# Optimization experiments

Hardware: AMD Instinct MI355X
Metric: run time of the kernel (lower is better)

## Reference

```python
import jax, jax.numpy as jnp
import numpy as np

# -------- static graph construction (Traffic4cast-style pixel grid) --------
H, W = 495, 436
N = H * W                    # 215820 nodes
D_NODE, D_EDGE, UNITS = 128, 32, 128
UQ = UNITS // 4              # per-quadrant width (combination='concat')
SCALE = 1.0 / 4.0            # 1/(max_neighbors+1)

def _first_occ_unique(v):
    """tf.unique semantics: unique values in first-occurrence order + idx map."""
    u, first, inv = np.unique(v, return_index=True, return_inverse=True)
    order = np.argsort(first)
    rank = np.empty(len(u), dtype=np.int64)
    rank[order] = np.arange(len(u))
    return u[order], rank[inv]

def _build_graph():
    r, c = np.meshgrid(np.arange(H), np.arange(W), indexing='ij')
    node_loc = np.stack([r.ravel(), c.ravel()], -1).astype(np.int64)
    def grid_edges(r0, r1, c0, c1, dr, dc):
        rr, cc = np.meshgrid(np.arange(r0, r1), np.arange(c0, c1), indexing='ij')
        src = (rr * W + cc).ravel()
        dst = ((rr + dr) * W + (cc + dc)).ravel()
        return np.stack([src, dst], -1).astype(np.int64)
    eis = [grid_edges(1, H, 0, W, -1, 0),   # north
           grid_edges(0, H, 0, W - 1, 0, 1),# east
           grid_edges(0, H - 1, 0, W, 1, 0),# south
           grid_edges(0, H, 1, W, 0, -1)]   # west
    return node_loc, eis

NODE_LOC, EIS = _build_graph()

# --- graph_pooling_2x2 bucketing (col_idx=0): pos_id = (r//2)*half_cols + c//2 ---
_half_cols = NODE_LOC[:, 0].max() + 1
_pos_id = (NODE_LOC // 2 * np.array([_half_cols, 1])).sum(-1)
_, NEW_NODE_IDS = _first_occ_unique(_pos_id)
N_POOLED = int(NEW_NODE_IDS.max()) + 1

# --- remove_duplicate_edges precompute per direction (static, int-only) ---
EDGE_SEG, K_UNIQ, KEEP_IDX, NEW_EIDX = [], [], [], []
for _ei in EIS:
    _pe = NEW_NODE_IDS[_ei]
    _lin = _pe[:, 0] * N + _pe[:, 1]
    _u, _seg = _first_occ_unique(_lin)
    _ne = np.stack([_u // N, _u % N], -1)
    _keep = np.where(_ne[:, 0] != _ne[:, 1])[0]
    EDGE_SEG.append(_seg)
    K_UNIQ.append(len(_u))
    KEEP_IDX.append(_keep)
    NEW_EIDX.append(_ne[_keep])


def setup_inputs() -> dict:
    key = jax.random.key(0)
    ks = jax.random.split(key, 9)
    inp = {
        'x': jax.random.normal(ks[0], (N, D_NODE), dtype=jnp.float32),
        'node_loc': jnp.asarray(NODE_LOC),
        'edge_index_n': jnp.asarray(EIS[0]),
        'edge_index_e': jnp.asarray(EIS[1]),
        'edge_index_s': jnp.asarray(EIS[2]),
        'edge_index_w': jnp.asarray(EIS[3]),
        'edges_n': jax.random.uniform(ks[1], (EIS[0].shape[0], D_EDGE), dtype=jnp.float32),
        'edges_e': jax.random.uniform(ks[2], (EIS[1].shape[0], D_EDGE), dtype=jnp.float32),
        'edges_s': jax.random.uniform(ks[3], (EIS[2].shape[0], D_EDGE), dtype=jnp.float32),
        'edges_w': jax.random.uniform(ks[4], (EIS[3].shape[0], D_EDGE), dtype=jnp.float32),
        'W_emb': jax.random.normal(ks[5], (4, D_NODE, UQ), dtype=jnp.float32) * 0.05,
        'W_edge': jax.random.normal(ks[6], (4, D_EDGE + 2 * UQ, UQ), dtype=jnp.float32) * 0.05,
        'W_node': jax.random.normal(ks[7], (D_NODE + UNITS, UNITS), dtype=jnp.float32) * 0.05,
    }
    return inp


def reference(x, node_loc, edge_index_n, edge_index_e, edge_index_s, edge_index_w,
              edges_n, edges_e, edges_s, edges_w, W_emb, W_edge, W_node):
    n = x.shape[0]
    eis = (edge_index_n, edge_index_e, edge_index_s, edge_index_w)
    efs = (edges_n, edges_e, edges_s, edges_w)
    aggs, quad_edges = [], []
    # GeoQuadrantGCN.call_concat (use_global=False, use_bias=False, relu)
    for q in range(4):
        ei = eis[q]
        xq = jax.nn.relu(x @ W_emb[q])                              # [N, UQ]
        edge_in = jnp.concatenate([efs[q], xq[ei[:, 0]], xq[ei[:, 1]]], axis=-1)
        edge = jax.nn.relu(edge_in @ W_edge[q])                     # [E, UQ]
        aggs.append(jax.ops.segment_sum(edge, ei[:, 1], num_segments=n) * SCALE)
        quad_edges.append(edge)
    x2 = jax.nn.relu(jnp.concatenate([x] + aggs, axis=-1) @ W_node) # [N, UNITS]
    # graph_pooling_2x2
    x_pooled = jax.ops.segment_max(x2, jnp.asarray(NEW_NODE_IDS), num_segments=N_POOLED)
    new_pos = jax.ops.segment_min(node_loc // 2, jnp.asarray(NEW_NODE_IDS), num_segments=N_POOLED)
    new_efeats = [
        jax.ops.segment_max(quad_edges[q], jnp.asarray(EDGE_SEG[q]), num_segments=K_UNIQ[q])[KEEP_IDX[q]]
        for q in range(4)
    ]
    new_eidx = [jnp.asarray(NEW_EIDX[q]) for q in range(4)]
    return (x_pooled, new_pos, *new_eidx, *new_efeats)
```

## Files before the change

kernel.cpp:

```cpp
#include <hip/hip_runtime.h>

#define NN 215820
#define NPOOL 54064
#define KN 53846
#define KE 53816

static constexpr size_t OFF_POS = (size_t)NPOOL * 128;
static constexpr size_t OFF_EIN = OFF_POS + (size_t)NPOOL * 2;
static constexpr size_t OFF_EIE = OFF_EIN + (size_t)KN * 2;
static constexpr size_t OFF_EIS = OFF_EIE + (size_t)KE * 2;
static constexpr size_t OFF_EIW = OFF_EIS + (size_t)KN * 2;
static constexpr size_t OFF_EFN = OFF_EIW + (size_t)KE * 2;
static constexpr size_t OFF_EFE = OFF_EFN + (size_t)KN * 32;
static constexpr size_t OFF_EFS = OFF_EFE + (size_t)KE * 32;
static constexpr size_t OFF_EFW = OFF_EFS + (size_t)KN * 32;

typedef __attribute__((ext_vector_type(8))) short  short8v;
typedef __attribute__((ext_vector_type(4))) float  floatx4;

__device__ __align__(16) unsigned short g_wn_h[128 * 256];
__device__ __align__(16) unsigned short g_wn_l[128 * 256];
__device__ __align__(16) unsigned short g_we_h[128 * 128];
__device__ __align__(16) unsigned short g_we_l[128 * 128];

__device__ __forceinline__ void bf16split(float x, unsigned short& h,
                                          unsigned short& l) {
  const unsigned int u = __float_as_uint(x);
  h = (unsigned short)(u >> 16);
  const float hf = __uint_as_float(u & 0xffff0000u);
  l = (unsigned short)(__float_as_uint(x - hf) >> 16);
}

__global__ __launch_bounds__(256, 4) void k_xq(const float* __restrict__ x,
                                               float* __restrict__ xq) {
  __shared__ __align__(16) short As_h[128 * 32], As_l[128 * 32];
  __shared__ __align__(16) short Bs_h[128 * 32], Bs_l[128 * 32];
  const int t  = threadIdx.x;
  const int n0 = blockIdx.x * 128;
  const int srow = t >> 1, q0 = t & 1;
  int sn = n0 + srow; if (sn >= NN) sn = NN - 1;
  const float* srcx = x + (size_t)sn * 128;
  const int w = t >> 6, lane = t & 63;
  const int lr = lane & 15, lg = lane >> 4;

  floatx4 acc[2][8];
#pragma unroll
  for (int mi = 0; mi < 2; ++mi)
#pragma unroll
    for (int ni = 0; ni < 8; ++ni) acc[mi][ni] = (floatx4){0.f, 0.f, 0.f, 0.f};

  for (int ks = 0; ks < 4; ++ks) {
    __syncthreads();
#pragma unroll
    for (int cc = 0; cc < 2; ++cc) {
      const int q = q0 + 2 * cc;
      const floatx4 v0 = *(const floatx4*)(srcx + ks * 32 + q * 8);
      const floatx4 v1 = *(const floatx4*)(srcx + ks * 32 + q * 8 + 4);
      short8v hv, lv;
#pragma unroll
      for (int j = 0; j < 4; ++j) {
        unsigned short h, l;
        bf16split(v0[j], h, l); hv[j] = (short)h; lv[j] = (short)l;
        bf16split(v1[j], h, l); hv[4 + j] = (short)h; lv[4 + j] = (short)l;
      }
      const int off = srow * 64 + ((q * 16) ^ ((srow & 3) << 4));
      *(short8v*)((char*)As_h + off) = hv;
      *(short8v*)((char*)As_l + off) = lv;
      const size_t wb = (size_t)srow * 128 + ks * 32 + q * 8;
      *(short8v*)((char*)Bs_h + off) = *(const short8v*)(g_we_h + wb);
      *(short8v*)((char*)Bs_l + off) = *(const short8v*)(g_we_l + wb);
    }
    __syncthreads();
    short8v ah[2], al[2];
#pragma unroll
    for (int mi = 0; mi < 2; ++mi) {
      const int row = (mi ? 64 : 0) + 16 * w + lr;
      const int off = row * 64 + ((lg * 16) ^ ((row & 3) << 4));
      ah[mi] = *(const short8v*)((const char*)As_h + off);
      al[mi] = *(const short8v*)((const char*)As_l + off);
    }
#pragma unroll
    for (int ni = 0; ni < 8; ++ni) {
      const int col = 16 * ni + lr;
      const int off = col * 64 + ((lg * 16) ^ ((col & 3) << 4));
      const short8v bh = *(const short8v*)((const char*)Bs_h + off);
      const short8v bl = *(const short8v*)((const char*)Bs_l + off);
#pragma unroll
      for (int mi = 0; mi < 2; ++mi) {
        acc[mi][ni] = __builtin_amdgcn_mfma_f32_16x16x32_bf16(ah[mi], bh, acc[mi][ni], 0, 0, 0);
        acc[mi][ni] = __builtin_amdgcn_mfma_f32_16x16x32_bf16(ah[mi], bl, acc[mi][ni], 0, 0, 0);
        acc[mi][ni] = __builtin_amdgcn_mfma_f32_16x16x32_bf16(al[mi], bh, acc[mi][ni], 0, 0, 0);
      }
    }
  }
#pragma unroll
  for (int ni = 0; ni < 8; ++ni) {
    const int col = 16 * ni + lr;
    const int qq = col >> 5, u = col & 31;
#pragma unroll
    for (int mi = 0; mi < 2; ++mi) {
      const int nb = n0 + (mi ? 64 : 0) + 16 * w + 4 * lg;
#pragma unroll
      for (int r = 0; r < 4; ++r) {
        const int n = nb + r;
        if (n < NN)
          xq[((size_t)qq * NN + n) * 32 + u] = fmaxf(acc[mi][ni][r], 0.f);
      }
    }
  }
}

__global__ __launch_bounds__(256, 4) void k_node(const float* __restrict__ x,
                                                 const float* __restrict__ agg,
                                                 float* __restrict__ out) {
  __shared__ short As_h[128 * 32], As_l[128 * 32];
  __shared__ short Bs_h[128 * 32], Bs_l[128 * 32];
  const int t   = threadIdx.x;
  const int pr  = blockIdx.y;
  const int pc0 = blockIdx.x * 32;

  const int srow = t >> 1, q0 = t & 1;
  int ra = (srow < 64) ? 2 * pr : 2 * pr + 1; if (ra > 494) ra = 494;
  int ca = 2 * pc0 + (srow & 63);          if (ca > 435) ca = 435;
  const size_t snode = (size_t)ra * 436 + ca;

  const int w = t >> 6, lane = t & 63;
  const int lr = lane & 15, lg = lane >> 4;

  floatx4 acc[2][8];
#pragma unroll
  for (int mi = 0; mi < 2; ++mi)
#pragma unroll
    for (int ni = 0; ni < 8; ++ni) acc[mi][ni] = (floatx4){0.f, 0.f, 0.f, 0.f};

  for (int ks = 0; ks < 8; ++ks) {
    __syncthreads();
    const float* src = (ks < 4) ? (x + snode * 128 + ks * 32)
                                : (agg + snode * 128 + (ks - 4) * 32);
#pragma unroll
    for (int cc = 0; cc < 2; ++cc) {
      const int q = q0 + 2 * cc;
      const floatx4 v0 = *(const floatx4*)(src + q * 8);
      const floatx4 v1 = *(const floatx4*)(src + q * 8 + 4);
      short8v hv, lv;
#pragma unroll
      for (int j = 0; j < 4; ++j) {
        unsigned short h, l;
        bf16split(v0[j], h, l); hv[j] = (short)h; lv[j] = (short)l;
        bf16split(v1[j], h, l); hv[4 + j] = (short)h; lv[4 + j] = (short)l;
      }
      const int off = srow * 64 + ((q * 16) ^ ((srow & 3) << 4));
      *(short8v*)((char*)As_h + off) = hv;
      *(short8v*)((char*)As_l + off) = lv;
      const size_t wb = (size_t)srow * 256 + ks * 32 + q * 8;
      *(short8v*)((char*)Bs_h + off) = *(const short8v*)(g_wn_h + wb);
      *(short8v*)((char*)Bs_l + off) = *(const short8v*)(g_wn_l + wb);
    }
    __syncthreads();
    short8v ah[2], al[2];
#pragma unroll
    for (int mi = 0; mi < 2; ++mi) {
      const int row = (mi ? 64 : 0) + 16 * w + lr;
      const int off = row * 64 + ((lg * 16) ^ ((row & 3) << 4));
      ah[mi] = *(const short8v*)((const char*)As_h + off);
      al[mi] = *(const short8v*)((const char*)As_l + off);
    }
#pragma unroll
    for (int ni = 0; ni < 8; ++ni) {
      const int col = 16 * ni + lr;
      const int off = col * 64 + ((lg * 16) ^ ((col & 3) << 4));
      const short8v bh = *(const short8v*)((const char*)Bs_h + off);
      const short8v bl = *(const short8v*)((const char*)Bs_l + off);
#pragma unroll
      for (int mi = 0; mi < 2; ++mi) {
        acc[mi][ni] = __builtin_amdgcn_mfma_f32_16x16x32_bf16(ah[mi], bh, acc[mi][ni], 0, 0, 0);
        acc[mi][ni] = __builtin_amdgcn_mfma_f32_16x16x32_bf16(ah[mi], bl, acc[mi][ni], 0, 0, 0);
        acc[mi][ni] = __builtin_amdgcn_mfma_f32_16x16x32_bf16(al[mi], bh, acc[mi][ni], 0, 0, 0);
      }
    }
  }
#pragma unroll
  for (int ni = 0; ni < 8; ++ni) {
#pragma unroll
    for (int k = 0; k < 2; ++k) {
      float v = fmaxf(fmaxf(acc[0][ni][2 * k], acc[0][ni][2 * k + 1]),
                      fmaxf(acc[1][ni][2 * k], acc[1][ni][2 * k + 1]));
      v = fmaxf(v, 0.f);
      const int pc = pc0 + 8 * w + 2 * lg + k;
      if (pc < 218) out[((size_t)pr * 218 + pc) * 128 + 16 * ni + lr] = v;
    }
  }
}

__global__ __launch_bounds__(256) void k_edge(
    const float* __restrict__ ef_n, const float* __restrict__ ef_e,
    const float* __restrict__ ef_s, const float* __restrict__ ef_w,
    const float* __restrict__ xq, const float* __restrict__ W_edge,
    float* __restrict__ agg, float* __restrict__ out) {
  const int q = blockIdx.y;
  const float* ef; float* efb; int P;
  if (q == 0)      { ef = ef_n; P = 107692; efb = out + OFF_EFN; }
  else if (q == 1) { ef = ef_e; P = 107880; efb = out + OFF_EFE; }
  else if (q == 2) { ef = ef_s; P = 107692; efb = out + OFF_EFS; }
  else             { ef = ef_w; P = 107880; efb = out + OFF_EFW; }
  const int j = threadIdx.x & 31, slot = threadIdx.x >> 5;
  const float* Wq = W_edge + q * 3072;
  float wcol[96];
#pragma unroll
  for (int k = 0; k < 96; ++k) wcol[k] = Wq[k * 32 + j];
  const float* xqq = xq + (size_t)q * NN * 32;
  __shared__ float ein[8][192];
  float* row = ein[slot];

  for (int p = blockIdx.x * 8 + slot; p < P; p += gridDim.x * 8) {
    int e1, src1, dst1, e2, src2, dst2, kidx; bool kept, has2;
    if (q == 0) {
      const int rp = p / 218, pc = p - rp * 218;
      const int r = rp + 1, c = 2 * pc;
      e1 = (r - 1) * 436 + c; e2 = e1 + 1;
      src1 = r * 436 + c; dst1 = src1 - 436;
      src2 = src1 + 1; dst2 = dst1 + 1; has2 = true;
      kept = (r & 1) == 0; kidx = ((r >> 1) - 1) * 218 + pc;
    } else if (q == 2) {
      const int r = p / 218, pc = p - r * 218;
      const int c = 2 * pc;
      e1 = r * 436 + c; e2 = e1 + 1;
      src1 = e1; dst1 = src1 + 436;
      src2 = src1 + 1; dst2 = dst1 + 1; has2 = true;
      kept = (r & 1) == 1; kidx = (r >> 1) * 218 + pc;
    } else if (q == 1) {
      const int pr = p / 435, c = p - pr * 435;
      e1 = 2 * pr * 435 + c; e2 = e1 + 435;
      src1 = 2 * pr * 436 + c; dst1 = src1 + 1;
      src2 = src1 + 436; dst2 = dst1 + 436;
      has2 = pr < 247;
      kept = (c & 1) == 1; kidx = pr * 217 + (c >> 1);
    } else {
      const int pr = p / 435, cm = p - pr * 435;
      const int c = cm + 1;
      e1 = 2 * pr * 435 + cm; e2 = e1 + 435;
      src1 = 2 * pr * 436 + c; dst1 = src1 - 1;
      src2 = src1 + 436; dst2 = dst1 + 436;
      has2 = pr < 247;
      kept = (c & 1) == 0; kidx = pr * 217 + (c >> 1) - 1;
    }
    const int e2c = has2 ? e2 : e1;
    const int s2c = has2 ? src2 : src1;
    const int d2c = has2 ? dst2 : dst1;
    row[j]       = ef[(size_t)e1 * 32 + j];
    row[32 + j]  = xqq[(size_t)src1 * 32 + j];
    row[64 + j]  = xqq[(size_t)dst1 * 32 + j];
    row[96 + j]  = ef[(size_t)e2c * 32 + j];
    row[128 + j] = xqq[(size_t)s2c * 32 + j];
    row[160 + j] = xqq[(size_t)d2c * 32 + j];
    float a1 = 0.f, a2 = 0.f;
#pragma unroll
    for (int kq = 0; kq < 24; ++kq) {
      const float4 b1 = *(const float4*)&row[4 * kq];
      const float4 b2 = *(const float4*)&row[96 + 4 * kq];
      a1 = fmaf(b1.x, wcol[4 * kq + 0], a1); a1 = fmaf(b1.y, wcol[4 * kq + 1], a1);
      a1 = fmaf(b1.z, wcol[4 * kq + 2], a1); a1 = fmaf(b1.w, wcol[4 * kq + 3], a1);
      a2 = fmaf(b2.x, wcol[4 * kq + 0], a2); a2 = fmaf(b2.y, wcol[4 * kq + 1], a2);
      a2 = fmaf(b2.z, wcol[4 * kq + 2], a2); a2 = fmaf(b2.w, wcol[4 * kq + 3], a2);
    }
    const float f1 = fmaxf(a1, 0.f), f2 = fmaxf(a2, 0.f);
    agg[(size_t)dst1 * 128 + q * 32 + j] = f1 * 0.25f;
    if (has2) agg[(size_t)dst2 * 128 + q * 32 + j] = f2 * 0.25f;
    if (kept) efb[(size_t)kidx * 32 + j] = has2 ? fmaxf(f1, f2) : f1;
  }
}

__global__ __launch_bounds__(256) void k_misc(float* __restrict__ out,
                                              float* __restrict__ agg,
                                              const float* __restrict__ W_node,
                                              const float* __restrict__ W_emb) {
  int u = blockIdx.x * 256 + threadIdx.x;
  if (u < 436 * 32) {
    agg[((size_t)494 * 436 + (u >> 5)) * 128 + (u & 31)] = 0.f; return;
  }
  u -= 436 * 32;
  if (u < 495 * 32) {
    agg[(size_t)(u >> 5) * 436 * 128 + 32 + (u & 31)] = 0.f; return;
  }
  u -= 495 * 32;
  if (u < 436 * 32) {
    agg[(size_t)(u >> 5) * 128 + 64 + (u & 31)] = 0.f; return;
  }
  u -= 436 * 32;
  if (u < 495 * 32) {
    agg[((size_t)(u >> 5) * 436 + 435) * 128 + 96 + (u & 31)] = 0.f; return;
  }
  u -= 495 * 32;
  if (u < NPOOL * 2) {
    const int p  = u >> 1;
    const int pr = p / 218, pc = p - pr * 218;
    out[OFF_POS + u] = (float)((u & 1) ? pc : pr); return;
  }
  u -= NPOOL * 2;
  if (u < KN * 2) {
    const int e  = u >> 1;
    const int kr = e / 218 + 1, pc = e - (kr - 1) * 218;
    const int s  = kr * 218 + pc;
    out[OFF_EIN + u] = (float)((u & 1) ? (s - 218) : s); return;
  }
  u -= KN * 2;
  if (u < KE * 2) {
    const int e  = u >> 1;
    const int pr = e / 217, jj = e - pr * 217;
    const int s  = pr * 218 + jj;
    out[OFF_EIE + u] = (float)((u & 1) ? (s + 1) : s); return;
  }
  u -= KE * 2;
  if (u < KN * 2) {
    const int e  = u >> 1;
    const int k  = e / 218, pc = e - k * 218;
    const int s  = k * 218 + pc;
    out[OFF_EIS + u] = (float)((u & 1) ? (s + 218) : s); return;
  }
  u -= KN * 2;
  if (u < KE * 2) {
    const int e  = u >> 1;
    const int pr = e / 217, jj = e - pr * 217;
    const int s  = pr * 218 + jj + 1;
    out[OFF_EIW + u] = (float)((u & 1) ? (s - 1) : s); return;
  }
  u -= KE * 2;
  if (u < 256 * 128) {
    const int k = u >> 7, c = u & 127;
    unsigned short h, l;
    bf16split(W_node[u], h, l);
    g_wn_h[(size_t)c * 256 + k] = h;
    g_wn_l[(size_t)c * 256 + k] = l;
    return;
  }
  u -= 256 * 128;
  if (u < 4 * 128 * 32) {
    const int q = u >> 12, k = (u >> 5) & 127, uu = u & 31;
    unsigned short h, l;
    bf16split(W_emb[u], h, l);
    g_we_h[(size_t)(q * 32 + uu) * 128 + k] = h;
    g_we_l[(size_t)(q * 32 + uu) * 128 + k] = l;
  }
}

extern "C" void kernel_launch(void* const* d_in, const int* in_sizes, int n_in,
                              void* d_out, int out_size, void* d_ws, size_t ws_size,
                              hipStream_t stream) {
  const float* x      = (const float*)d_in[0];
  const float* ef_n   = (const float*)d_in[6];
  const float* ef_e   = (const float*)d_in[7];
  const float* ef_s   = (const float*)d_in[8];
  const float* ef_w   = (const float*)d_in[9];
  const float* W_emb  = (const float*)d_in[10];
  const float* W_edge = (const float*)d_in[11];
  const float* W_node = (const float*)d_in[12];
  float* out = (float*)d_out;

  float* xq  = (float*)d_ws;
  float* agg = xq + (size_t)NN * 128;

  const int misc_total = (436 + 495 + 436 + 495) * 32 + NPOOL * 2 +
                         2 * (KN * 2 + KE * 2) + 256 * 128 + 4 * 128 * 32;
  k_misc<<<dim3((misc_total + 255) / 256), 256, 0, stream>>>(out, agg,
                                                             W_node, W_emb);
  k_xq  <<<dim3((NN + 127) / 128), 256, 0, stream>>>(x, xq);
  k_edge<<<dim3(512, 4), 256, 0, stream>>>(ef_n, ef_e, ef_s, ef_w,
                                           xq, W_edge, agg, out);
  k_node<<<dim3(7, 248), 256, 0, stream>>>(x, agg, out);
}
```

Measured before the change: 467.0 us.

## Rewrite edge MLP as split-bf16 MFMA GEMM over spatial tiles

Replaces the scalar per-edge FMA loop in the edge kernel with a tiled 128x32x96 GEMM on MFMA. It splits fp32 into high and low bf16 halves and issues three products to keep near-fp32 accuracy. The W_edge matrix is pre-split into bf16 halves in the misc kernel. Edges are now tiled by grid rows and columns so gathers are contiguous and the pooled max is done in registers. This targets the FP32 ALU cost and the shared-memory row staging, at the price of more blocks, conversion work and redundant overlapping tiles at row ends.

Measured after the change: 448.8 us. 3.9% less time.

```diff
diff --git a/kernel.cpp b/kernel.cpp
--- a/kernel.cpp
+++ b/kernel.cpp
@@ -22,6 +22,8 @@
 __device__ __align__(16) unsigned short g_wn_l[128 * 256];
 __device__ __align__(16) unsigned short g_we_h[128 * 128];
 __device__ __align__(16) unsigned short g_we_l[128 * 128];
+__device__ __align__(16) unsigned short g_wd_h[128 * 96];
+__device__ __align__(16) unsigned short g_wd_l[128 * 96];
 
 __device__ __forceinline__ void bf16split(float x, unsigned short& h,
                                           unsigned short& l) {
@@ -192,88 +194,178 @@
   }
 }
 
-__global__ __launch_bounds__(256) void k_edge(
+__global__ __launch_bounds__(256, 4) void k_edge(
     const float* __restrict__ ef_n, const float* __restrict__ ef_e,
     const float* __restrict__ ef_s, const float* __restrict__ ef_w,
-    const float* __restrict__ xq, const float* __restrict__ W_edge,
-    float* __restrict__ agg, float* __restrict__ out) {
-  const int q = blockIdx.y;
-  const float* ef; float* efb; int P;
-  if (q == 0)      { ef = ef_n; P = 107692; efb = out + OFF_EFN; }
-  else if (q == 1) { ef = ef_e; P = 107880; efb = out + OFF_EFE; }
-  else if (q == 2) { ef = ef_s; P = 107692; efb = out + OFF_EFS; }
-  else             { ef = ef_w; P = 107880; efb = out + OFF_EFW; }
-  const int j = threadIdx.x & 31, slot = threadIdx.x >> 5;
-  const float* Wq = W_edge + q * 3072;
-  float wcol[96];
-#pragma unroll
-  for (int k = 0; k < 96; ++k) wcol[k] = Wq[k * 32 + j];
+    const float* __restrict__ xq, float* __restrict__ agg,
+    float* __restrict__ out) {
+  __shared__ __align__(16) short As_h[128 * 32], As_l[128 * 32];
+  __shared__ __align__(16) short Bs_h[32 * 32],  Bs_l[32 * 32];
+  const int t = threadIdx.x;
+  int b = blockIdx.x;
+
+  int q, row = 0, pr = 0, c0;
+  const float* ef; float* efb;
+  if (b < 1976)        { q = 0; ef = ef_n; efb = out + OFF_EFN;
+                         row = b >> 2; c0 = (b & 3) * 128; if (c0 > 308) c0 = 308; }
+  else if (b < 3952)   { b -= 1976; q = 2; ef = ef_s; efb = out + OFF_EFS;
+                         row = b >> 2; c0 = (b & 3) * 128; if (c0 > 308) c0 = 308; }
+  else if (b < 5688)   { b -= 3952; q = 1; ef = ef_e; efb = out + OFF_EFE;
+                         pr = b / 7;  c0 = (b - pr * 7) * 64; if (c0 > 371) c0 = 371; }
+  else                 { b -= 5688; q = 3; ef = ef_w; efb = out + OFF_EFW;
+                         pr = b / 7;  c0 = (b - pr * 7) * 64; if (c0 > 371) c0 = 371; }
   const float* xqq = xq + (size_t)q * NN * 32;
-  __shared__ float ein[8][192];
-  float* row = ein[slot];
-
-  for (int p = blockIdx.x * 8 + slot; p < P; p += gridDim.x * 8) {
-    int e1, src1, dst1, e2, src2, dst2, kidx; bool kept, has2;
-    if (q == 0) {
-      const int rp = p / 218, pc = p - rp * 218;
-      const int r = rp + 1, c = 2 * pc;
-      e1 = (r - 1) * 436 + c; e2 = e1 + 1;
-      src1 = r * 436 + c; dst1 = src1 - 436;
-      src2 = src1 + 1; dst2 = dst1 + 1; has2 = true;
-      kept = (r & 1) == 0; kidx = ((r >> 1) - 1) * 218 + pc;
-    } else if (q == 2) {
-      const int r = p / 218, pc = p - r * 218;
-      const int c = 2 * pc;
-      e1 = r * 436 + c; e2 = e1 + 1;
-      src1 = e1; dst1 = src1 + 436;
-      src2 = src1 + 1; dst2 = dst1 + 1; has2 = true;
-      kept = (r & 1) == 1; kidx = (r >> 1) * 218 + pc;
-    } else if (q == 1) {
-      const int pr = p / 435, c = p - pr * 435;
-      e1 = 2 * pr * 435 + c; e2 = e1 + 435;
-      src1 = 2 * pr * 436 + c; dst1 = src1 + 1;
-      src2 = src1 + 436; dst2 = dst1 + 436;
-      has2 = pr < 247;
-      kept = (c & 1) == 1; kidx = pr * 217 + (c >> 1);
+
+  const int srow = t >> 1, q0 = t & 1;
+  const float *base0, *base1, *base2;
+  if (q == 0) {
+    const int e = row * 436 + c0 + srow;
+    base0 = ef  + (size_t)e * 32;
+    base1 = xqq + (size_t)(e + 436) * 32;
+    base2 = xqq + (size_t)e * 32;
+  } else if (q == 2) {
+    const int e = row * 436 + c0 + srow;
+    base0 = ef  + (size_t)e * 32;
+    base1 = xqq + (size_t)e * 32;
+    base2 = xqq + (size_t)(e + 436) * 32;
+  } else {
+    int r = 2 * pr + (srow >> 6); if (r > 494) r = 494;
+    const int cc = c0 + (srow & 63);
+    if (q == 1) {
+      base0 = ef  + ((size_t)r * 435 + cc) * 32;
+      base1 = xqq + ((size_t)r * 436 + cc) * 32;
+      base2 = base1 + 32;
     } else {
-      const int pr = p / 435, cm = p - pr * 435;
-      const int c = cm + 1;
-      e1 = 2 * pr * 435 + cm; e2 = e1 + 435;
-      src1 = 2 * pr * 436 + c; dst1 = src1 - 1;
-      src2 = src1 + 436; dst2 = dst1 + 436;
-      has2 = pr < 247;
-      kept = (c & 1) == 0; kidx = pr * 217 + (c >> 1) - 1;
-    }
-    const int e2c = has2 ? e2 : e1;
-    const int s2c = has2 ? src2 : src1;
-    const int d2c = has2 ? dst2 : dst1;
-    row[j]       = ef[(size_t)e1 * 32 + j];
-    row[32 + j]  = xqq[(size_t)src1 * 32 + j];
-    row[64 + j]  = xqq[(size_t)dst1 * 32 + j];
-    row[96 + j]  = ef[(size_t)e2c * 32 + j];
-    row[128 + j] = xqq[(size_t)s2c * 32 + j];
-    row[160 + j] = xqq[(size_t)d2c * 32 + j];
-    float a1 = 0.f, a2 = 0.f;
-#pragma unroll
-    for (int kq = 0; kq < 24; ++kq) {
-      const float4 b1 = *(const float4*)&row[4 * kq];
-      const float4 b2 = *(const float4*)&row[96 + 4 * kq];
-      a1 = fmaf(b1.x, wcol[4 * kq + 0], a1); a1 = fmaf(b1.y, wcol[4 * kq + 1], a1);
-      a1 = fmaf(b1.z, wcol[4 * kq + 2], a1); a1 = fmaf(b1.w, wcol[4 * kq + 3], a1);
-      a2 = fmaf(b2.x, wcol[4 * kq + 0], a2); a2 = fmaf(b2.y, wcol[4 * kq + 1], a2);
-      a2 = fmaf(b2.z, wcol[4 * kq + 2], a2); a2 = fmaf(b2.w, wcol[4 * kq + 3], a2);
-    }
-    const float f1 = fmaxf(a1, 0.f), f2 = fmaxf(a2, 0.f);
-    agg[(size_t)dst1 * 128 + q * 32 + j] = f1 * 0.25f;
-    if (has2) agg[(size_t)dst2 * 128 + q * 32 + j] = f2 * 0.25f;
-    if (kept) efb[(size_t)kidx * 32 + j] = has2 ? fmaxf(f1, f2) : f1;
+      base0 = ef  + ((size_t)r * 435 + cc) * 32;
+      base1 = xqq + ((size_t)r * 436 + cc + 1) * 32;
+      base2 = base1 - 32;
+    }
+  }
+
+  const int w = t >> 6, lane = t & 63;
+  const int lr = lane & 15, lg = lane >> 4;
+
+  floatx4 acc[2][2];
+#pragma unroll
+  for (int mi = 0; mi < 2; ++mi)
+#pragma unroll
+    for (int ni = 0; ni < 2; ++ni) acc[mi][ni] = (floatx4){0.f, 0.f, 0.f, 0.f};
+
+  for (int kc = 0; kc < 3; ++kc) {
+    __syncthreads();
+    const float* src = (kc == 0) ? base0 : (kc == 1) ? base1 : base2;
+#pragma unroll
+    for (int cc = 0; cc < 2; ++cc) {
+      const int qch = q0 + 2 * cc;
+      const floatx4 v0 = *(const floatx4*)(src + qch * 8);
+      const floatx4 v1 = *(const floatx4*)(src + qch * 8 + 4);
+      short8v hv, lv;
+#pragma unroll
+      for (int j = 0; j < 4; ++j) {
+        unsigned short h, l;
+        bf16split(v0[j], h, l); hv[j] = (short)h; lv[j] = (short)l;
+        bf16split(v1[j], h, l); hv[4 + j] = (short)h; lv[4 + j] = (short)l;
+      }
+      const int off = srow * 64 + ((qch * 16) ^ ((srow & 3) << 4));
+      *(short8v*)((char*)As_h + off) = hv;
+      *(short8v*)((char*)As_l + off) = lv;
+    }
+    if (t < 128) {
+      const int col = t >> 2, ch = t & 3;
+      const size_t wb = (size_t)(q * 32 + col) * 96 + kc * 32 + ch * 8;
+      const int off = col * 64 + ((ch * 16) ^ ((col & 3) << 4));
+      *(short8v*)((char*)Bs_h + off) = *(const short8v*)(g_wd_h + wb);
+      *(short8v*)((char*)Bs_l + off) = *(const short8v*)(g_wd_l + wb);
+    }
+    __syncthreads();
+    short8v ah[2], al[2], bh[2], bl[2];
+#pragma unroll
+    for (int mi = 0; mi < 2; ++mi) {
+      const int rowm = 64 * mi + 16 * w + lr;
+      const int off = rowm * 64 + ((lg * 16) ^ ((rowm & 3) << 4));
+      ah[mi] = *(const short8v*)((const char*)As_h + off);
+      al[mi] = *(const short8v*)((const char*)As_l + off);
+    }
+#pragma unroll
+    for (int ni = 0; ni < 2; ++ni) {
+      const int col = 16 * ni + lr;
+      const int off = col * 64 + ((lg * 16) ^ ((col & 3) << 4));
+      bh[ni] = *(const short8v*)((const char*)Bs_h + off);
+      bl[ni] = *(const short8v*)((const char*)Bs_l + off);
+    }
+#pragma unroll
+    for (int ni = 0; ni < 2; ++ni)
+#pragma unroll
+      for (int mi = 0; mi < 2; ++mi) {
+        acc[mi][ni] = __builtin_amdgcn_mfma_f32_16x16x32_bf16(ah[mi], bh[ni], acc[mi][ni], 0, 0, 0);
+        acc[mi][ni] = __builtin_amdgcn_mfma_f32_16x16x32_bf16(ah[mi], bl[ni], acc[mi][ni], 0, 0, 0);
+        acc[mi][ni] = __builtin_amdgcn_mfma_f32_16x16x32_bf16(al[mi], bh[ni], acc[mi][ni], 0, 0, 0);
+      }
+  }
+
+  float vv[2][2][4];
+#pragma unroll
+  for (int mi = 0; mi < 2; ++mi)
+#pragma unroll
+    for (int ni = 0; ni < 2; ++ni)
+#pragma unroll
+      for (int r = 0; r < 4; ++r) vv[mi][ni][r] = fmaxf(acc[mi][ni][r], 0.f);
+
+#pragma unroll
+  for (int ni = 0; ni < 2; ++ni) {
+    const int colo = q * 32 + 16 * ni + lr;
+#pragma unroll
+    for (int mi = 0; mi < 2; ++mi) {
+      size_t dstb;
+      if (q == 0)      dstb = (size_t)row * 436 + c0 + 64 * mi + 16 * w + 4 * lg;
+      else if (q == 2) dstb = (size_t)(row + 1) * 436 + c0 + 64 * mi + 16 * w + 4 * lg;
+      else {
+        int r2 = 2 * pr + mi; if (r2 > 494) r2 = 494;
+        dstb = (size_t)r2 * 436 + c0 + 16 * w + 4 * lg + (q == 1 ? 1 : 0);
+      }
+#pragma unroll
+      for (int r = 0; r < 4; ++r)
+        agg[(dstb + r) * 128 + colo] = vv[mi][ni][r] * 0.25f;
+    }
+  }
+
+  if (q == 0 || q == 2) {
+    if (row & 1) {
+      const int krow = row >> 1;
+#pragma unroll
+      for (int ni = 0; ni < 2; ++ni)
+#pragma unroll
+        for (int mi = 0; mi < 2; ++mi)
+#pragma unroll
+          for (int k = 0; k < 2; ++k) {
+            const int c = c0 + 64 * mi + 16 * w + 4 * lg + 2 * k;
+            const int kidx = krow * 218 + (c >> 1);
+            const float val = fmaxf(vv[mi][ni][2 * k], vv[mi][ni][2 * k + 1]);
+            efb[(size_t)kidx * 32 + 16 * ni + lr] = val;
+          }
+    }
+  } else {
+#pragma unroll
+    for (int ni = 0; ni < 2; ++ni)
+#pragma unroll
+      for (int r = 0; r < 4; ++r) {
+        const int jj = 16 * w + 4 * lg + r;
+        const int c = c0 + jj + (q == 3 ? 1 : 0);
+        const bool kept = (q == 1) ? ((c & 1) == 1) : ((c & 1) == 0);
+        if (kept) {
+          const int kidx = pr * 217 + (c >> 1) - (q == 3 ? 1 : 0);
+          const float val = fmaxf(vv[0][ni][r], vv[1][ni][r]);
+          efb[(size_t)kidx * 32 + 16 * ni + lr] = val;
+        }
+      }
   }
 }
 
 __global__ __launch_bounds__(256) void k_misc(float* __restrict__ out,
                                               float* __restrict__ agg,
                                               const float* __restrict__ W_node,
-                                              const float* __restrict__ W_emb) {
+                                              const float* __restrict__ W_emb,
+                                              const float* __restrict__ W_edge) {
   int u = blockIdx.x * 256 + threadIdx.x;
   if (u < 436 * 32) {
     agg[((size_t)494 * 436 + (u >> 5)) * 128 + (u & 31)] = 0.f; return;
@@ -340,6 +432,16 @@
     bf16split(W_emb[u], h, l);
     g_we_h[(size_t)(q * 32 + uu) * 128 + k] = h;
     g_we_l[(size_t)(q * 32 + uu) * 128 + k] = l;
+    return;
+  }
+  u -= 4 * 128 * 32;
+  if (u < 4 * 96 * 32) {
+    const int q = u / 3072, rem = u - q * 3072;
+    const int k = rem >> 5, col = rem & 31;
+    unsigned short h, l;
+    bf16split(W_edge[u], h, l);
+    g_wd_h[(size_t)(q * 32 + col) * 96 + k] = h;
+    g_wd_l[(size_t)(q * 32 + col) * 96 + k] = l;
   }
 }
 
@@ -360,11 +462,12 @@
   float* agg = xq + (size_t)NN * 128;
 
   const int misc_total = (436 + 495 + 436 + 495) * 32 + NPOOL * 2 +
-                         2 * (KN * 2 + KE * 2) + 256 * 128 + 4 * 128 * 32;
-  k_misc<<<dim3((misc_total + 255) / 256), 256, 0, stream>>>(out, agg,
-                                                             W_node, W_emb);
+                         2 * (KN * 2 + KE * 2) + 256 * 128 + 4 * 128 * 32 +
+                         4 * 96 * 32;
+  k_misc<<<dim3((misc_total + 255) / 256), 256, 0, stream>>>(out, agg, W_node,
+                                                             W_emb, W_edge);
   k_xq  <<<dim3((NN + 127) / 128), 256, 0, stream>>>(x, xq);
-  k_edge<<<dim3(512, 4), 256, 0, stream>>>(ef_n, ef_e, ef_s, ef_w,
-                                           xq, W_edge, agg, out);
+  k_edge<<<dim3(7424), 256, 0, stream>>>(ef_n, ef_e, ef_s, ef_w,
+                                         xq, agg, out);
   k_node<<<dim3(7, 248), 256, 0, stream>>>(x, agg, out);
 }
```
